# Kernel tuning notes

Measured on AMD Instinct MI355X. Metric: run time of the kernel, lower is better.

The kernel has to match this reference:

```python
import jax, jax.numpy as jnp
import numpy as np

EPS = 1e-7
N_NODES = 100000

# --- Lorentz model (c = 1), working at the origin o = (1, 0, ..., 0) ---

def expmap0(v_spatial):
    """Exp map at origin: tangent spatial part [N, d] -> hyperboloid point [N, d+1]."""
    nrm = jnp.sqrt(jnp.maximum(jnp.sum(v_spatial * v_spatial, axis=-1, keepdims=True), EPS))
    x0 = jnp.cosh(nrm)
    xs = jnp.sinh(nrm) / nrm * v_spatial
    return jnp.concatenate([x0, xs], axis=-1)


def logmap0(x):
    """Log map at origin: point [N, d+1] -> tangent spatial part [N, d]."""
    x0 = jnp.maximum(x[..., :1], 1.0 + EPS)
    xs = x[..., 1:]
    nrm = jnp.sqrt(jnp.maximum(jnp.sum(xs * xs, axis=-1, keepdims=True), EPS))
    return jnp.arccosh(x0) / nrm * xs


def sigmoid_nonlin(x):
    # log map -> sigmoid in tangent space -> exp map (c_in = c_out = 1)
    return expmap0(jax.nn.sigmoid(logmap0(x)))


def hgcn_layer(x, edge_index, W, b):
    """HGCN conv: tangent-space linear + mean aggregation over edges + exp map."""
    t = logmap0(x)                      # [N, d_in]
    h = t @ W + b                       # [N, d_out]
    src, dst = edge_index[0], edge_index[1]
    msg = h[src]                        # [E, d_out] gather
    agg = jax.ops.segment_sum(msg, dst, num_segments=N_NODES)
    deg = jax.ops.segment_sum(jnp.ones((edge_index.shape[1],), h.dtype), dst,
                              num_segments=N_NODES)
    agg = agg / jnp.maximum(deg, 1.0)[:, None]
    return expmap0(agg)


def setup_inputs() -> dict:
    key = jax.random.key(0)
    ks = jax.random.split(key, 10)
    d_in, h1, h2, h_mlp, d_out = 64, 64, 64, 128, 40
    return {
        "features": jax.random.normal(ks[0], (N_NODES, d_in), jnp.float32),
        "edge_index": jax.random.randint(ks[1], (2, 1600000), 0, N_NODES, jnp.int64),
        "W1": jax.random.normal(ks[2], (d_in, h1), jnp.float32) * 0.05,
        "b1": jnp.zeros((h1,), jnp.float32),
        "W2": jax.random.normal(ks[3], (h1, h2), jnp.float32) * 0.05,
        "b2": jnp.zeros((h2,), jnp.float32),
        "W3": jax.random.normal(ks[4], (h2, h_mlp), jnp.float32) * 0.05,
        "b3": jnp.zeros((h_mlp,), jnp.float32),
        "W4": jax.random.normal(ks[5], (h_mlp, d_out), jnp.float32) * 0.05,
        "b4": jnp.zeros((d_out,), jnp.float32),
    }


def reference(features, edge_index, W1, b1, W2, b2, W3, b3, W4, b4):
    # lift Euclidean features to the hyperboloid (pad time coord, exp map)
    x = expmap0(features)                       # [N, d_in+1]
    x = hgcn_layer(x, edge_index, W1, b1)
    x = sigmoid_nonlin(x)
    x = hgcn_layer(x, edge_index, W2, b2)
    x = sigmoid_nonlin(x)
    t = logmap0(x)                              # [N, h2] (spatial part, drops time coord)
    # MLP head (dropout inactive at eval)
    h = jax.nn.relu(t @ W3 + b3)
    return h @ W4 + b4
```

## Files before the change

kernel.cpp:

```cpp
#include <hip/hip_runtime.h>


constexpr int CSHIFT = 9;
constexpr int CNODES = 1 << CSHIFT;
constexpr int EPB    = 4096;
constexpr int EPT    = EPB / 256;
constexpr int CAP    = 16384;

constexpr int W1F_OFF = 0;
constexpr int W2F_OFF = 4096;
constexpr int W3F_OFF = 8192;
constexpr int W4F_OFF = 16384;
constexpr int WIMG_TOT = 22528;

typedef __attribute__((ext_vector_type(8))) short short8;
typedef __attribute__((ext_vector_type(4))) float floatx4;

__device__ __forceinline__ float sigmoidf(float x) {
    return 1.0f / (1.0f + __expf(-x));
}
__device__ __forceinline__ unsigned short f2bf(float f) {
    unsigned int u = __float_as_uint(f);
    u = (u + 0x7FFFu + ((u >> 16) & 1u)) >> 16;
    return (unsigned short)u;
}

__global__ __launch_bounds__(256) void prep_cast_k(
    const float* __restrict__ feat, unsigned short* __restrict__ featbf,
    const float* __restrict__ W1, const float* __restrict__ W2,
    const float* __restrict__ W3, const float* __restrict__ W4,
    unsigned short* __restrict__ img, int n8)
{
    int i = blockIdx.x * 256 + threadIdx.x;
    if (i < n8) {
        const float4* p = (const float4*)feat + (size_t)i * 2;
        float4 a = p[0], b = p[1];
        uint4 o;
        o.x = (unsigned)f2bf(a.x) | ((unsigned)f2bf(a.y) << 16);
        o.y = (unsigned)f2bf(a.z) | ((unsigned)f2bf(a.w) << 16);
        o.z = (unsigned)f2bf(b.x) | ((unsigned)f2bf(b.y) << 16);
        o.w = (unsigned)f2bf(b.z) | ((unsigned)f2bf(b.w) << 16);
        ((uint4*)featbf)[i] = o;
        return;
    }
    int t = i - n8;
    if (t >= WIMG_TOT) return;
    float v = 0.f;
    int s = t;
    if (s < W2F_OFF) {
        int j = s & 7, m = (s >> 3) & 15, q = (s >> 7) & 3, kk = (s >> 9) & 1, c = s >> 10;
        v = W1[(kk * 32 + q * 8 + j) * 64 + c * 16 + m];
    } else if (s < W3F_OFF) {
        s -= W2F_OFF;
        int j = s & 7, m = (s >> 3) & 15, q = (s >> 7) & 3, kk = (s >> 9) & 1, c = s >> 10;
        v = W2[(kk * 32 + q * 8 + j) * 64 + c * 16 + m];
    } else if (s < W4F_OFF) {
        s -= W3F_OFF;
        int j = s & 7, m = (s >> 3) & 15, q = (s >> 7) & 3, kk = (s >> 9) & 1, c = s >> 10;
        v = W3[(kk * 32 + q * 8 + j) * 128 + c * 16 + m];
    } else {
        s -= W4F_OFF;
        int j = s & 7, m = (s >> 3) & 15, q = (s >> 7) & 3, kk = (s >> 9) & 3, c = s >> 11;
        int n = c * 16 + m;
        if (n < 40) v = W4[(kk * 32 + q * 8 + j) * 40 + n];
    }
    img[t] = f2bf(v);
}

__global__ __launch_bounds__(256) void part_a(const int* __restrict__ src,
                                              const int* __restrict__ dst,
                                              int* __restrict__ ccur,
                                              int* __restrict__ arena,
                                              int E, int NBUCK) {
    __shared__ int  hist[256];
    __shared__ int  exoff[256];
    __shared__ int  lcur[256];
    __shared__ int  gbase[256];
    __shared__ int  stage[EPB];
    __shared__ unsigned char stageB[EPB];

    const int tid = threadIdx.x;
    const int e0  = blockIdx.x * EPB;
    const int ec  = min(EPB, E - e0);

    int pk[EPT], bk[EPT];
    hist[tid] = 0;
    __syncthreads();
    #pragma unroll
    for (int j = 0; j < EPT; j++) {
        int idx = tid + j * 256;
        if (idx < ec) {
            int s = src[e0 + idx];
            int d = dst[e0 + idx];
            bk[j] = d >> CSHIFT;
            pk[j] = s | ((d & (CNODES - 1)) << 17);
            atomicAdd(&hist[bk[j]], 1);
        } else bk[j] = -1;
    }
    __syncthreads();
    const int h = hist[tid];
    exoff[tid] = h;
    __syncthreads();
    for (int dd = 1; dd < 256; dd <<= 1) {
        int v = 0;
        if (tid >= dd) v = exoff[tid - dd];
        __syncthreads();
        if (tid >= dd) exoff[tid] += v;
        __syncthreads();
    }
    const int ex = exoff[tid] - h;
    int gb = 0;
    if (tid < NBUCK && h > 0) gb = atomicAdd(ccur + tid, h);
    __syncthreads();
    exoff[tid] = ex;
    lcur[tid]  = ex;
    gbase[tid] = gb;
    __syncthreads();
    #pragma unroll
    for (int j = 0; j < EPT; j++) {
        if (bk[j] >= 0) {
            int l = atomicAdd(&lcur[bk[j]], 1);
            stage[l]  = pk[j];
            stageB[l] = (unsigned char)bk[j];
        }
    }
    __syncthreads();
    for (int i = tid; i < ec; i += 256) {
        int b = stageB[i];
        arena[(size_t)b * CAP + gbase[b] + (i - exoff[b])] = stage[i];
    }
}

__global__ __launch_bounds__(256) void csr_fine(const int* __restrict__ arena,
                                                const int* __restrict__ ccur,
                                                int* __restrict__ off,
                                                int* __restrict__ ssrc,
                                                int N, int E, int NBUCK) {
    __shared__ int cnt[CNODES];
    __shared__ int cur[CNODES];
    __shared__ int part[256];
    const int b = blockIdx.x;
    const int node0 = b << CSHIFT;
    const int tid = threadIdx.x;

    part[tid] = (tid < NBUCK) ? ccur[tid] : 0;
    __syncthreads();
    for (int d = 1; d < 256; d <<= 1) {
        int v = 0;
        if (tid >= d) v = part[tid - d];
        __syncthreads();
        if (tid >= d) part[tid] += v;
        __syncthreads();
    }
    const int cbeg = (b > 0) ? part[b - 1] : 0;
    const int ec   = ccur[b];
    if (b == 0 && tid == 0) off[N] = E;
    __syncthreads();

    const int* pe = arena + (size_t)b * CAP;
    cnt[tid] = 0;
    cnt[tid + 256] = 0;
    __syncthreads();
    for (int i = tid; i < ec; i += 256)
        atomicAdd(&cnt[(pe[i] >> 17) & (CNODES - 1)], 1);
    __syncthreads();
    const int c0 = cnt[2 * tid], c1 = cnt[2 * tid + 1];
    part[tid] = c0 + c1;
    __syncthreads();
    for (int d = 1; d < 256; d <<= 1) {
        int v = 0;
        if (tid >= d) v = part[tid - d];
        __syncthreads();
        if (tid >= d) part[tid] += v;
        __syncthreads();
    }
    const int ex = (tid > 0) ? part[tid - 1] : 0;
    cur[2 * tid]     = ex;
    cur[2 * tid + 1] = ex + c0;
    if (node0 + 2 * tid     < N) off[node0 + 2 * tid]     = cbeg + ex;
    if (node0 + 2 * tid + 1 < N) off[node0 + 2 * tid + 1] = cbeg + ex + c0;
    __syncthreads();
    for (int i = tid; i < ec; i += 256) {
        int p = pe[i];
        int pos = cbeg + atomicAdd(&cur[(p >> 17) & (CNODES - 1)], 1);
        ssrc[pos] = p & 0x1FFFF;
    }
}

#define ACC8(v)                                    \
    acc[0] += __uint_as_float((v).x << 16);        \
    acc[1] += __uint_as_float((v).x & 0xFFFF0000u);\
    acc[2] += __uint_as_float((v).y << 16);        \
    acc[3] += __uint_as_float((v).y & 0xFFFF0000u);\
    acc[4] += __uint_as_float((v).z << 16);        \
    acc[5] += __uint_as_float((v).z & 0xFFFF0000u);\
    acc[6] += __uint_as_float((v).w << 16);        \
    acc[7] += __uint_as_float((v).w & 0xFFFF0000u);

__device__ __forceinline__ void gather_tile(
    const unsigned short* __restrict__ h, const int* __restrict__ off,
    const int* __restrict__ ssrc, unsigned short* Agg, int rowB, int N, int tid)
{
    #pragma unroll
    for (int pass = 0; pass < 2; pass++) {
        int rl = pass * 32 + (tid >> 3);
        int g  = rowB + rl;
        int q  = (tid & 7) * 8;
        uint4 p = make_uint4(0u, 0u, 0u, 0u);
        if (g < N) {
            int beg = off[g], end = off[g + 1];
            float acc[8] = {0.f, 0.f, 0.f, 0.f, 0.f, 0.f, 0.f, 0.f};
            int i = beg;
            for (; i + 8 <= end; i += 8) {
                uint4 v0 = *(const uint4*)(h + (size_t)ssrc[i]     * 64 + q);
                uint4 v1 = *(const uint4*)(h + (size_t)ssrc[i + 1] * 64 + q);
                uint4 v2 = *(const uint4*)(h + (size_t)ssrc[i + 2] * 64 + q);
                uint4 v3 = *(const uint4*)(h + (size_t)ssrc[i + 3] * 64 + q);
                uint4 v4 = *(const uint4*)(h + (size_t)ssrc[i + 4] * 64 + q);
                uint4 v5 = *(const uint4*)(h + (size_t)ssrc[i + 5] * 64 + q);
                uint4 v6 = *(const uint4*)(h + (size_t)ssrc[i + 6] * 64 + q);
                uint4 v7 = *(const uint4*)(h + (size_t)ssrc[i + 7] * 64 + q);
                ACC8(v0); ACC8(v1); ACC8(v2); ACC8(v3);
                ACC8(v4); ACC8(v5); ACC8(v6); ACC8(v7);
            }
            for (; i + 2 <= end; i += 2) {
                uint4 v0 = *(const uint4*)(h + (size_t)ssrc[i]     * 64 + q);
                uint4 v1 = *(const uint4*)(h + (size_t)ssrc[i + 1] * 64 + q);
                ACC8(v0); ACC8(v1);
            }
            for (; i < end; i++) {
                uint4 v = *(const uint4*)(h + (size_t)ssrc[i] * 64 + q);
                ACC8(v);
            }
            float inv = 1.0f / (float)max(end - beg, 1);
            p.x = (unsigned)f2bf(acc[0]*inv) | ((unsigned)f2bf(acc[1]*inv) << 16);
            p.y = (unsigned)f2bf(acc[2]*inv) | ((unsigned)f2bf(acc[3]*inv) << 16);
            p.z = (unsigned)f2bf(acc[4]*inv) | ((unsigned)f2bf(acc[5]*inv) << 16);
            p.w = (unsigned)f2bf(acc[6]*inv) | ((unsigned)f2bf(acc[7]*inv) << 16);
        }
        *(uint4*)(Agg + rl * 72 + q) = p;
    }
}

__global__ __launch_bounds__(256) void aggemm1_k(
    const unsigned short* __restrict__ featbf, const int* __restrict__ off,
    const int* __restrict__ ssrc, const unsigned short* __restrict__ img,
    const float* __restrict__ bias, unsigned short* __restrict__ t1, int N)
{
    __shared__ alignas(16) unsigned short Agg[64 * 72];

    const int tid = threadIdx.x;
    const int rowB = blockIdx.x * 64;
    gather_tile(featbf, off, ssrc, Agg, rowB, N, tid);
    __syncthreads();

    const int w = tid >> 6, lane = tid & 63;
    const int m = lane & 15, quad = lane >> 4;
    const int row0 = rowB + w * 16;
    const short8* Wf = (const short8*)(img + W1F_OFF);

    floatx4 acc[4];
    #pragma unroll
    for (int c = 0; c < 4; c++) acc[c] = (floatx4){0.f, 0.f, 0.f, 0.f};
    #pragma unroll
    for (int kk = 0; kk < 2; kk++) {
        short8 a = *(const short8*)(Agg + (w * 16 + m) * 72 + kk * 32 + quad * 8);
        #pragma unroll
        for (int c = 0; c < 4; c++) {
            short8 b = Wf[((c * 2 + kk) * 4 + quad) * 16 + m];
            acc[c] = __builtin_amdgcn_mfma_f32_16x16x32_bf16(a, b, acc[c], 0, 0, 0);
        }
    }
    bool dzr[4];
    int rows[4];
    #pragma unroll
    for (int r = 0; r < 4; r++) {
        rows[r] = row0 + quad * 4 + r;
        dzr[r] = (rows[r] < N) ? (off[rows[r] + 1] == off[rows[r]]) : false;
    }
    #pragma unroll
    for (int c = 0; c < 4; c++) {
        int col = c * 16 + m;
        float bv = bias[col];
        #pragma unroll
        for (int r = 0; r < 4; r++) {
            if (rows[r] < N) {
                float v = dzr[r] ? 0.5f : sigmoidf(acc[c][r] + bv);
                t1[(size_t)rows[r] * 64 + col] = f2bf(v);
            }
        }
    }
}

__global__ __launch_bounds__(256) void aggep3_k(
    const unsigned short* __restrict__ t1, const int* __restrict__ off,
    const int* __restrict__ ssrc, const unsigned short* __restrict__ img,
    const float* __restrict__ b2, const float* __restrict__ b3,
    const float* __restrict__ b4, float* __restrict__ out, int N)
{
    __shared__ alignas(16) unsigned short SM[13312];
    unsigned short* T2  = SM;
    unsigned short* Agg = SM + 4608;
    unsigned short* H3  = SM + 4608;

    const int tid = threadIdx.x;
    const int rowB = blockIdx.x * 64;
    gather_tile(t1, off, ssrc, Agg, rowB, N, tid);
    __syncthreads();

    const int w = tid >> 6, lane = tid & 63;
    const int m = lane & 15, quad = lane >> 4;
    const int row0 = rowB + w * 16;

    {
        const short8* Wf = (const short8*)(img + W2F_OFF);
        floatx4 acc[4];
        #pragma unroll
        for (int c = 0; c < 4; c++) acc[c] = (floatx4){0.f, 0.f, 0.f, 0.f};
        #pragma unroll
        for (int kk = 0; kk < 2; kk++) {
            short8 a = *(const short8*)(Agg + (w * 16 + m) * 72 + kk * 32 + quad * 8);
            #pragma unroll
            for (int c = 0; c < 4; c++) {
                short8 b = Wf[((c * 2 + kk) * 4 + quad) * 16 + m];
                acc[c] = __builtin_amdgcn_mfma_f32_16x16x32_bf16(a, b, acc[c], 0, 0, 0);
            }
        }
        bool dzr[4];
        #pragma unroll
        for (int r = 0; r < 4; r++) {
            int row = row0 + quad * 4 + r;
            dzr[r] = (row < N) ? (off[row + 1] == off[row]) : false;
        }
        __syncthreads();
        #pragma unroll
        for (int c = 0; c < 4; c++) {
            int col = c * 16 + m;
            float bv = b2[col];
            #pragma unroll
            for (int r = 0; r < 4; r++) {
                int rl = w * 16 + quad * 4 + r;
                float v = dzr[r] ? 0.5f : sigmoidf(acc[c][r] + bv);
                T2[rl * 72 + col] = f2bf(v);
            }
        }
    }
    __syncthreads();

    {
        const short8* Wf = (const short8*)(img + W3F_OFF);
        floatx4 acc[8];
        #pragma unroll
        for (int c = 0; c < 8; c++) acc[c] = (floatx4){0.f, 0.f, 0.f, 0.f};
        #pragma unroll
        for (int kk = 0; kk < 2; kk++) {
            short8 a = *(const short8*)(T2 + (w * 16 + m) * 72 + kk * 32 + quad * 8);
            #pragma unroll
            for (int c = 0; c < 8; c++) {
                short8 b = Wf[((c * 2 + kk) * 4 + quad) * 16 + m];
                acc[c] = __builtin_amdgcn_mfma_f32_16x16x32_bf16(a, b, acc[c], 0, 0, 0);
            }
        }
        #pragma unroll
        for (int c = 0; c < 8; c++) {
            int col = c * 16 + m;
            float bv = b3[col];
            #pragma unroll
            for (int r = 0; r < 4; r++) {
                int rl = w * 16 + quad * 4 + r;
                H3[rl * 136 + col] = f2bf(fmaxf(acc[c][r] + bv, 0.f));
            }
        }
    }
    __syncthreads();

    {
        const short8* Wf = (const short8*)(img + W4F_OFF);
        floatx4 acc[3];
        #pragma unroll
        for (int c = 0; c < 3; c++) acc[c] = (floatx4){0.f, 0.f, 0.f, 0.f};
        #pragma unroll
        for (int kk = 0; kk < 4; kk++) {
            short8 a = *(const short8*)(H3 + (w * 16 + m) * 136 + kk * 32 + quad * 8);
            #pragma unroll
            for (int c = 0; c < 3; c++) {
                short8 b = Wf[((c * 4 + kk) * 4 + quad) * 16 + m];
                acc[c] = __builtin_amdgcn_mfma_f32_16x16x32_bf16(a, b, acc[c], 0, 0, 0);
            }
        }
        #pragma unroll
        for (int c = 0; c < 3; c++) {
            int col = c * 16 + m;
            if (col < 40) {
                float bv = b4[col];
                #pragma unroll
                for (int r = 0; r < 4; r++) {
                    int row = row0 + quad * 4 + r;
                    if (row < N) out[(size_t)row * 40 + col] = acc[c][r] + bv;
                }
            }
        }
    }
}

extern "C" void kernel_launch(void* const* d_in, const int* in_sizes, int n_in,
                              void* d_out, int out_size, void* d_ws, size_t ws_size,
                              hipStream_t stream)
{
    const float* feat = (const float*)d_in[0];
    const int*   eidx = (const int*)d_in[1];
    const float* W1 = (const float*)d_in[2];
    const float* b1 = (const float*)d_in[3];
    const float* W2 = (const float*)d_in[4];
    const float* b2 = (const float*)d_in[5];
    const float* W3 = (const float*)d_in[6];
    const float* b3 = (const float*)d_in[7];
    const float* W4 = (const float*)d_in[8];
    const float* b4 = (const float*)d_in[9];

    const int N = in_sizes[0] / 64;
    const int E = in_sizes[1] / 2;
    const int* src = eidx;
    const int* dst = eidx + E;

    const int NBUCK = (N + CNODES - 1) / CNODES;

    unsigned short* featbf = (unsigned short*)d_ws;
    unsigned short* t1     = featbf + (size_t)N * 64;
    unsigned short* img    = t1     + (size_t)N * 64;
    int*   off   = (int*)(img + WIMG_TOT);
    int*   ccur  = off + (N + 1);
    int*   ssrc  = ccur + NBUCK;
    int*   arena = ssrc + E;
    float* out   = (float*)d_out;

    hipMemsetAsync(ccur, 0, (size_t)NBUCK * sizeof(int), stream);

    const dim3 blk(256);
    const int gP  = (E + EPB - 1) / EPB;
    const int g64 = (N + 63) / 64;
    const int n8  = N * 64 / 8;
    const int gPC = (n8 + WIMG_TOT + 255) / 256;

    prep_cast_k<<<gPC, blk, 0, stream>>>(feat, featbf, W1, W2, W3, W4, img, n8);
    part_a<<<gP, blk, 0, stream>>>(src, dst, ccur, arena, E, NBUCK);
    csr_fine<<<NBUCK, blk, 0, stream>>>(arena, ccur, off, ssrc, N, E, NBUCK);

    aggemm1_k<<<g64, blk, 0, stream>>>(featbf, off, ssrc, img, b1, t1, N);
    aggep3_k<<<g64, blk, 0, stream>>>(t1, off, ssrc, img, b2, b3, b4, out, N);
}
```

Measured before the change: 234.6 us.

## Merge prep and partition kernels; make gather per-wave and split MLP head

```diff
diff --git a/kernel.cpp b/kernel.cpp
--- a/kernel.cpp
+++ b/kernel.cpp
@@ -25,53 +25,14 @@
     return (unsigned short)u;
 }
 
-__global__ __launch_bounds__(256) void prep_cast_k(
+__global__ __launch_bounds__(256) void part_prep_k(
+    const int* __restrict__ src, const int* __restrict__ dst,
+    int* __restrict__ ccur, int* __restrict__ arena, int E, int NBUCK, int gP,
     const float* __restrict__ feat, unsigned short* __restrict__ featbf,
     const float* __restrict__ W1, const float* __restrict__ W2,
     const float* __restrict__ W3, const float* __restrict__ W4,
     unsigned short* __restrict__ img, int n8)
 {
-    int i = blockIdx.x * 256 + threadIdx.x;
-    if (i < n8) {
-        const float4* p = (const float4*)feat + (size_t)i * 2;
-        float4 a = p[0], b = p[1];
-        uint4 o;
-        o.x = (unsigned)f2bf(a.x) | ((unsigned)f2bf(a.y) << 16);
-        o.y = (unsigned)f2bf(a.z) | ((unsigned)f2bf(a.w) << 16);
-        o.z = (unsigned)f2bf(b.x) | ((unsigned)f2bf(b.y) << 16);
-        o.w = (unsigned)f2bf(b.z) | ((unsigned)f2bf(b.w) << 16);
-        ((uint4*)featbf)[i] = o;
-        return;
-    }
-    int t = i - n8;
-    if (t >= WIMG_TOT) return;
-    float v = 0.f;
-    int s = t;
-    if (s < W2F_OFF) {
-        int j = s & 7, m = (s >> 3) & 15, q = (s >> 7) & 3, kk = (s >> 9) & 1, c = s >> 10;
-        v = W1[(kk * 32 + q * 8 + j) * 64 + c * 16 + m];
-    } else if (s < W3F_OFF) {
-        s -= W2F_OFF;
-        int j = s & 7, m = (s >> 3) & 15, q = (s >> 7) & 3, kk = (s >> 9) & 1, c = s >> 10;
-        v = W2[(kk * 32 + q * 8 + j) * 64 + c * 16 + m];
-    } else if (s < W4F_OFF) {
-        s -= W3F_OFF;
-        int j = s & 7, m = (s >> 3) & 15, q = (s >> 7) & 3, kk = (s >> 9) & 1, c = s >> 10;
-        v = W3[(kk * 32 + q * 8 + j) * 128 + c * 16 + m];
-    } else {
-        s -= W4F_OFF;
-        int j = s & 7, m = (s >> 3) & 15, q = (s >> 7) & 3, kk = (s >> 9) & 3, c = s >> 11;
-        int n = c * 16 + m;
-        if (n < 40) v = W4[(kk * 32 + q * 8 + j) * 40 + n];
-    }
-    img[t] = f2bf(v);
-}
-
-__global__ __launch_bounds__(256) void part_a(const int* __restrict__ src,
-                                              const int* __restrict__ dst,
-                                              int* __restrict__ ccur,
-                                              int* __restrict__ arena,
-                                              int E, int NBUCK) {
     __shared__ int  hist[256];
     __shared__ int  exoff[256];
     __shared__ int  lcur[256];
@@ -80,6 +41,45 @@
     __shared__ unsigned char stageB[EPB];
 
     const int tid = threadIdx.x;
+
+    if ((int)blockIdx.x >= gP) {
+        int i = ((int)blockIdx.x - gP) * 256 + tid;
+        if (i < n8) {
+            const float4* p = (const float4*)feat + (size_t)i * 2;
+            float4 a = p[0], b = p[1];
+            uint4 o;
+            o.x = (unsigned)f2bf(a.x) | ((unsigned)f2bf(a.y) << 16);
+            o.y = (unsigned)f2bf(a.z) | ((unsigned)f2bf(a.w) << 16);
+            o.z = (unsigned)f2bf(b.x) | ((unsigned)f2bf(b.y) << 16);
+            o.w = (unsigned)f2bf(b.z) | ((unsigned)f2bf(b.w) << 16);
+            ((uint4*)featbf)[i] = o;
+            return;
+        }
+        int t = i - n8;
+        if (t >= WIMG_TOT) return;
+        float v = 0.f;
+        int s = t;
+        if (s < W2F_OFF) {
+            int j = s & 7, m = (s >> 3) & 15, q = (s >> 7) & 3, kk = (s >> 9) & 1, c = s >> 10;
+            v = W1[(kk * 32 + q * 8 + j) * 64 + c * 16 + m];
+        } else if (s < W3F_OFF) {
+            s -= W2F_OFF;
+            int j = s & 7, m = (s >> 3) & 15, q = (s >> 7) & 3, kk = (s >> 9) & 1, c = s >> 10;
+            v = W2[(kk * 32 + q * 8 + j) * 64 + c * 16 + m];
+        } else if (s < W4F_OFF) {
+            s -= W3F_OFF;
+            int j = s & 7, m = (s >> 3) & 15, q = (s >> 7) & 3, kk = (s >> 9) & 1, c = s >> 10;
+            v = W3[(kk * 32 + q * 8 + j) * 128 + c * 16 + m];
+        } else {
+            s -= W4F_OFF;
+            int j = s & 7, m = (s >> 3) & 15, q = (s >> 7) & 3, kk = (s >> 9) & 3, c = s >> 11;
+            int n = c * 16 + m;
+            if (n < 40) v = W4[(kk * 32 + q * 8 + j) * 40 + n];
+        }
+        img[t] = f2bf(v);
+        return;
+    }
+
     const int e0  = blockIdx.x * EPB;
     const int ec  = min(EPB, E - e0);
 
@@ -197,15 +197,16 @@
     acc[6] += __uint_as_float((v).w << 16);        \
     acc[7] += __uint_as_float((v).w & 0xFFFF0000u);
 
-__device__ __forceinline__ void gather_tile(
+__device__ __forceinline__ void gather_tile_wave(
     const unsigned short* __restrict__ h, const int* __restrict__ off,
-    const int* __restrict__ ssrc, unsigned short* Agg, int rowB, int N, int tid)
+    const int* __restrict__ ssrc, unsigned short* Agg, int rowB, int N,
+    int w, int lane)
 {
     #pragma unroll
     for (int pass = 0; pass < 2; pass++) {
-        int rl = pass * 32 + (tid >> 3);
+        int rl = w * 16 + pass * 8 + (lane >> 3);
         int g  = rowB + rl;
-        int q  = (tid & 7) * 8;
+        int q  = (lane & 7) * 8;
         uint4 p = make_uint4(0u, 0u, 0u, 0u);
         if (g < N) {
             int beg = off[g], end = off[g + 1];
@@ -251,14 +252,13 @@
 
     const int tid = threadIdx.x;
     const int rowB = blockIdx.x * 64;
-    gather_tile(featbf, off, ssrc, Agg, rowB, N, tid);
-    __syncthreads();
-
     const int w = tid >> 6, lane = tid & 63;
     const int m = lane & 15, quad = lane >> 4;
     const int row0 = rowB + w * 16;
+
+    gather_tile_wave(featbf, off, ssrc, Agg, rowB, N, w, lane);
+
     const short8* Wf = (const short8*)(img + W1F_OFF);
-
     floatx4 acc[4];
     #pragma unroll
     for (int c = 0; c < 4; c++) acc[c] = (floatx4){0.f, 0.f, 0.f, 0.f};
@@ -298,20 +298,19 @@
     const float* __restrict__ b2, const float* __restrict__ b3,
     const float* __restrict__ b4, float* __restrict__ out, int N)
 {
-    __shared__ alignas(16) unsigned short SM[13312];
+    __shared__ alignas(16) unsigned short SM[9216];
     unsigned short* T2  = SM;
     unsigned short* Agg = SM + 4608;
-    unsigned short* H3  = SM + 4608;
+    unsigned short* H3h = SM + 4608;
 
     const int tid = threadIdx.x;
     const int rowB = blockIdx.x * 64;
-    gather_tile(t1, off, ssrc, Agg, rowB, N, tid);
-    __syncthreads();
-
     const int w = tid >> 6, lane = tid & 63;
     const int m = lane & 15, quad = lane >> 4;
     const int row0 = rowB + w * 16;
 
+    gather_tile_wave(t1, off, ssrc, Agg, rowB, N, w, lane);
+
     {
         const short8* Wf = (const short8*)(img + W2F_OFF);
         floatx4 acc[4];
@@ -332,7 +331,6 @@
             int row = row0 + quad * 4 + r;
             dzr[r] = (row < N) ? (off[row + 1] == off[row]) : false;
         }
-        __syncthreads();
         #pragma unroll
         for (int c = 0; c < 4; c++) {
             int col = c * 16 + m;
@@ -345,59 +343,57 @@
             }
         }
     }
-    __syncthreads();
-
-    {
-        const short8* Wf = (const short8*)(img + W3F_OFF);
-        floatx4 acc[8];
-        #pragma unroll
-        for (int c = 0; c < 8; c++) acc[c] = (floatx4){0.f, 0.f, 0.f, 0.f};
+
+    floatx4 acc2[3];
+    #pragma unroll
+    for (int c = 0; c < 3; c++) acc2[c] = (floatx4){0.f, 0.f, 0.f, 0.f};
+    const short8* Wf3 = (const short8*)(img + W3F_OFF);
+    const short8* Wf4 = (const short8*)(img + W4F_OFF);
+
+    #pragma unroll
+    for (int half = 0; half < 2; half++) {
+        floatx4 acc[4];
+        #pragma unroll
+        for (int c = 0; c < 4; c++) acc[c] = (floatx4){0.f, 0.f, 0.f, 0.f};
         #pragma unroll
         for (int kk = 0; kk < 2; kk++) {
             short8 a = *(const short8*)(T2 + (w * 16 + m) * 72 + kk * 32 + quad * 8);
             #pragma unroll
-            for (int c = 0; c < 8; c++) {
-                short8 b = Wf[((c * 2 + kk) * 4 + quad) * 16 + m];
+            for (int c = 0; c < 4; c++) {
+                short8 b = Wf3[(((half * 4 + c) * 2 + kk) * 4 + quad) * 16 + m];
                 acc[c] = __builtin_amdgcn_mfma_f32_16x16x32_bf16(a, b, acc[c], 0, 0, 0);
             }
         }
         #pragma unroll
-        for (int c = 0; c < 8; c++) {
+        for (int c = 0; c < 4; c++) {
             int col = c * 16 + m;
-            float bv = b3[col];
+            float bv = b3[half * 64 + col];
             #pragma unroll
             for (int r = 0; r < 4; r++) {
                 int rl = w * 16 + quad * 4 + r;
-                H3[rl * 136 + col] = f2bf(fmaxf(acc[c][r] + bv, 0.f));
-            }
-        }
-    }
-    __syncthreads();
-
-    {
-        const short8* Wf = (const short8*)(img + W4F_OFF);
-        floatx4 acc[3];
-        #pragma unroll
-        for (int c = 0; c < 3; c++) acc[c] = (floatx4){0.f, 0.f, 0.f, 0.f};
-        #pragma unroll
-        for (int kk = 0; kk < 4; kk++) {
-            short8 a = *(const short8*)(H3 + (w * 16 + m) * 136 + kk * 32 + quad * 8);
+                H3h[rl * 72 + col] = f2bf(fmaxf(acc[c][r] + bv, 0.f));
+            }
+        }
+        #pragma unroll
+        for (int kk2 = 0; kk2 < 2; kk2++) {
+            short8 a = *(const short8*)(H3h + (w * 16 + m) * 72 + kk2 * 32 + quad * 8);
             #pragma unroll
             for (int c = 0; c < 3; c++) {
-                short8 b = Wf[((c * 4 + kk) * 4 + quad) * 16 + m];
-                acc[c] = __builtin_amdgcn_mfma_f32_16x16x32_bf16(a, b, acc[c], 0, 0, 0);
-            }
-        }
-        #pragma unroll
-        for (int c = 0; c < 3; c++) {
-            int col = c * 16 + m;
-            if (col < 40) {
-                float bv = b4[col];
-                #pragma unroll
-                for (int r = 0; r < 4; r++) {
-                    int row = row0 + quad * 4 + r;
-                    if (row < N) out[(size_t)row * 40 + col] = acc[c][r] + bv;
-                }
+                short8 b = Wf4[((c * 4 + half * 2 + kk2) * 4 + quad) * 16 + m];
+                acc2[c] = __builtin_amdgcn_mfma_f32_16x16x32_bf16(a, b, acc2[c], 0, 0, 0);
+            }
+        }
+    }
+
+    #pragma unroll
+    for (int c = 0; c < 3; c++) {
+        int col = c * 16 + m;
+        if (col < 40) {
+            float bv = b4[col];
+            #pragma unroll
+            for (int r = 0; r < 4; r++) {
+                int row = row0 + quad * 4 + r;
+                if (row < N) out[(size_t)row * 40 + col] = acc2[c][r] + bv;
             }
         }
     }
@@ -442,8 +438,9 @@
     const int n8  = N * 64 / 8;
     const int gPC = (n8 + WIMG_TOT + 255) / 256;
 
-    prep_cast_k<<<gPC, blk, 0, stream>>>(feat, featbf, W1, W2, W3, W4, img, n8);
-    part_a<<<gP, blk, 0, stream>>>(src, dst, ccur, arena, E, NBUCK);
+    part_prep_k<<<gP + gPC, blk, 0, stream>>>(src, dst, ccur, arena, E, NBUCK,
+                                              gP, feat, featbf, W1, W2, W3, W4,
+                                              img, n8);
     csr_fine<<<NBUCK, blk, 0, stream>>>(arena, ccur, off, ssrc, N, E, NBUCK);
 
     aggemm1_k<<<g64, blk, 0, stream>>>(featbf, off, ssrc, img, b1, t1, N);
```

New measurement: 226.9 us. 1.03x faster.
